# Performance work log

Measured on AMD Instinct MI355X. Metric: run time of the kernel, lower is better.

The kernel has to match this reference:

```python
import jax, jax.numpy as jnp
import numpy as np

# Module dims (match init_kwargs / input_specs)
V = 25        # number of graph nodes (chain skeleton)
K = 3         # max receptive-field size (neighbors incl. self), padded
CIN = 64
COUT = 64
N = 16
T = 512
TK = 3        # temporal_kernel
PAD = TK // 2 # time_pad default


def _build_graph():
    # Chain adjacency with self-links: node i <-> {i-1, i, i+1}
    A = np.zeros((V, V), np.float32)
    for i in range(V):
        A[i, i] = 1.0
        if i > 0:
            A[i, i - 1] = 1.0
        if i < V - 1:
            A[i, i + 1] = 1.0
    # Pad each node's neighbor list to K entries; mask marks real neighbors.
    idx = np.zeros((V, K), np.int32)
    mask = np.zeros((V, K), bool)
    for i in range(V):
        nb = np.where(A[i] != 0)[0]
        idx[i, : len(nb)] = nb
        mask[i, : len(nb)] = True
    return idx, mask


def setup_inputs() -> dict:
    key = jax.random.key(0)
    k_x, k_w, k_b = jax.random.split(key, 3)
    x = jax.random.normal(k_x, (N, CIN, V, T), dtype=jnp.float32)
    # One Conv2d kernel per node: [V, C_out, C_in, K, TK]; padded neighbor
    # slots are zeroed via mask inside reference().
    W = jax.random.normal(k_w, (V, COUT, CIN, K, TK), dtype=jnp.float32) * 0.05
    b = jax.random.normal(k_b, (V, COUT), dtype=jnp.float32) * 0.05
    idx_np, mask_np = _build_graph()
    return {
        "x": x,
        "W": W,
        "b": b,
        "idx": jnp.asarray(idx_np),
        "mask": jnp.asarray(mask_np),
    }


def reference(x, W, b, idx, mask):
    # x: [N, C, V, T]; W: [V, O, C, K, TK]; b: [V, O]; idx/mask: [V, K]
    Tt = x.shape[-1]
    # Zero out padded neighbor slots so padded rows contribute nothing
    # (equivalent to torch's variable-height per-node kernels).
    Wm = jnp.where(mask[:, None, None, :, None], W, 0.0)
    # Temporal zero padding (Conv2d padding=(0, time_pad))
    xp = jnp.pad(x, ((0, 0), (0, 0), (0, 0), (PAD, PAD)))
    # Batched neighbor gather: [N, C, V, K, T + 2*PAD]
    g = xp[:, :, idx, :]
    # Cross-correlation over the TK temporal taps (stride 1)
    out = jnp.zeros((x.shape[0], W.shape[1], V, Tt), dtype=x.dtype)
    for kt in range(TK):
        out = out + jnp.einsum(
            "ncvkt,vock->novt", g[..., kt : kt + Tt], Wm[..., kt]
        )
    out = out + b.T[None, :, :, None]  # per-node bias [O, V]
    return out
```

## Files before the change

### kernel.cpp

```cpp
#include <hip/hip_runtime.h>
#include <hip/hip_bf16.h>

#define NB   16
#define CINC 64
#define COUTC 64
#define NV   25
#define TLEN 512
#define KK   3
#define TKK  3

typedef short short8 __attribute__((ext_vector_type(8)));
typedef float f32x4  __attribute__((ext_vector_type(4)));
typedef float f32x16 __attribute__((ext_vector_type(16)));

#define XT_ROWS 514
#define XS_STRIDE 17408
#define NWT3BLK (NV * 9)

__device__ __forceinline__ unsigned pack_bf16(float lo, float hi) {
  __hip_bfloat16 l = __float2bfloat16(lo);
  __hip_bfloat16 h = __float2bfloat16(hi);
  unsigned short ul = *reinterpret_cast<unsigned short*>(&l);
  unsigned short uh = *reinterpret_cast<unsigned short*>(&h);
  return (unsigned)ul | ((unsigned)uh << 16);
}

__global__ __launch_bounds__(256) void prep_all(
    const float* __restrict__ x, const float* __restrict__ W,
    const unsigned char* __restrict__ mask_raw,
    __hip_bfloat16* __restrict__ Wt3, __hip_bfloat16* __restrict__ xT) {
  __shared__ float ts[64][65];
  int bid = blockIdx.x;
  if (bid < NWT3BLK) {
    int blk = bid;
    int v = blk / 9, kkt = blk % 9, k = kkt / 3, kt = kkt % 3;
    const int* mi = (const int*)mask_raw;
    int ok = 1;
    for (int i = 0; i < 18; ++i) {
      int m = mi[i];
      if (m != 0 && m != 1) ok = 0;
    }
    int m = ok ? mi[v * KK + k] : (int)(mask_raw[v * KK + k] != 0);
    const float* Wv = W + (size_t)v * COUTC * CINC * 9;
    __hip_bfloat16* dst = Wt3 + (size_t)blk * 4096;
    for (int i = threadIdx.x; i < 4096; i += 256) {
      int e     = i & 7;
      int lane  = (i >> 3) & 63;
      int ks    = (i >> 9) & 3;
      int oslab = i >> 11;
      int o = oslab * 32 + (lane & 31);
      int c = ks * 16 + 8 * (lane >> 5) + e;
      float val = m ? Wv[(o * CINC + c) * 9 + k * 3 + kt] : 0.f;
      dst[i] = __float2bfloat16(val);
    }
    return;
  }
  bid -= NWT3BLK;
  const int tb = (bid & 7) * 64;
  const int vn = bid >> 3;
  const int v  = vn % NV;
  const int n  = vn / NV;
  const int tid = threadIdx.x;
  for (int i = tid; i < 1024; i += 256) {
    int c = i >> 4, tq = (i & 15) * 4;
    float4 val = *(const float4*)(x + (((size_t)n * CINC + c) * NV + v) * TLEN + tb + tq);
    ts[c][tq + 0] = val.x;
    ts[c][tq + 1] = val.y;
    ts[c][tq + 2] = val.z;
    ts[c][tq + 3] = val.w;
  }
  __syncthreads();
  unsigned* base = (unsigned*)(xT + ((size_t)(n * NV + v) * XT_ROWS) * CINC);
  for (int i = tid; i < 512; i += 256) {
    int c8 = i & 7, t = i >> 3;
    int c0 = c8 * 8;
    uint4 d;
    d.x = pack_bf16(ts[c0 + 0][t], ts[c0 + 1][t]);
    d.y = pack_bf16(ts[c0 + 2][t], ts[c0 + 3][t]);
    d.z = pack_bf16(ts[c0 + 4][t], ts[c0 + 5][t]);
    d.w = pack_bf16(ts[c0 + 6][t], ts[c0 + 7][t]);
    *(uint4*)(base + (size_t)(tb + 1 + t) * 32 + c8 * 4) = d;
  }
  if (tb == 0 && tid < 32) base[tid] = 0u;
  if (tb == TLEN - 64 && tid < 32) base[513 * 32 + tid] = 0u;
}

__device__ __forceinline__ const char* slab_base(const __hip_bfloat16* xT,
                                                 int n, int vk, int tb) {
  return (const char*)xT + ((size_t)(n * NV + vk) * XT_ROWS + tb) * 128;
}

__global__ __launch_bounds__(256, 2) void lcn_mfma32(
    const __hip_bfloat16* __restrict__ xT,
    const __hip_bfloat16* __restrict__ Wt3,
    const float* __restrict__ bias,
    const int* __restrict__ idx,
    float* __restrict__ out) {
  __shared__ char xs[KK][XS_STRIDE];
  __shared__ char xs_dummy[1024];

  const int b  = blockIdx.x;
  const int n  = b & 15;
  const int tc = (b >> 4) & 1;
  const int v  = b >> 5;
  const int tid  = threadIdx.x;
  const int lane = tid & 63;
  const int wave = tid >> 6;
  const int os   = wave & 1;
  const int th   = wave >> 1;
  const int hi   = lane >> 5;
  const int l31  = lane & 31;

#define STAGE_PHASE(TBP)                                                      \
  {                                                                           \
    const char* gbs[KK] = {                                                   \
        slab_base(xT, n, idx[v * KK + 0], (TBP)),                             \
        slab_base(xT, n, idx[v * KK + 1], (TBP)),                             \
        slab_base(xT, n, idx[v * KK + 2], (TBP))};                            \
    _Pragma("unroll") for (int s = 0; s < KK; ++s) {                          \
      const char* gb = gbs[s];                                                \
      _Pragma("unroll") for (int q = 0; q < 4; ++q) {                         \
        int c = wave + q * 4;                                                 \
        int Lb = c * 1024 + lane * 16;                                        \
        int g = Lb ^ (((Lb >> 7) & 7) << 4);                                  \
        __builtin_amdgcn_global_load_lds(                                     \
            (const __attribute__((address_space(1))) void*)(gb + g),          \
            (__attribute__((address_space(3))) void*)(&xs[s][c * 1024]),      \
            16, 0, 0);                                                        \
      }                                                                       \
      if (wave == 0) {                                                        \
        int Lb = 16 * 1024 + lane * 16;                                       \
        int g = Lb ^ (((Lb >> 7) & 7) << 4);                                  \
        __builtin_amdgcn_global_load_lds(                                     \
            (const __attribute__((address_space(1))) void*)(gb + g),          \
            (__attribute__((address_space(3))) void*)(&xs[s][16 * 1024]),     \
            16, 0, 0);                                                        \
      } else {                                                                \
        __builtin_amdgcn_global_load_lds(                                     \
            (const __attribute__((address_space(1))) void*)(gb + lane * 16),  \
            (__attribute__((address_space(3))) void*)(xs_dummy),              \
            16, 0, 0);                                                        \
      }                                                                       \
      __builtin_amdgcn_sched_barrier(0);                                      \
    }                                                                         \
  }

#define COMPUTE_K(CB, KB)                                                     \
  _Pragma("unroll") for (int kt = 0; kt < TKK; ++kt) {                        \
    {                                                                         \
      const int r  = th * 64 + l31 + kt;                                      \
      const int sw = (r & 7) << 4;                                            \
      const int co = hi * 16;                                                 \
      const char* bp = (CB) + r * 128;                                        \
      _Pragma("unroll") for (int ks = 0; ks < 4; ++ks) {                      \
        short8 bfr = *(const short8*)(bp + ((co + 32 * ks) ^ sw));            \
        acc0 = __builtin_amdgcn_mfma_f32_32x32x16_bf16(                       \
            aA[((KB) + kt) * 4 + ks], bfr, acc0, 0, 0, 0);                    \
      }                                                                       \
    }                                                                         \
    {                                                                         \
      const int r  = th * 64 + 32 + l31 + kt;                                 \
      const int sw = (r & 7) << 4;                                            \
      const int co = hi * 16;                                                 \
      const char* bp = (CB) + r * 128;                                        \
      _Pragma("unroll") for (int ks = 0; ks < 4; ++ks) {                      \
        short8 bfr = *(const short8*)(bp + ((co + 32 * ks) ^ sw));            \
        acc1 = __builtin_amdgcn_mfma_f32_32x32x16_bf16(                       \
            aA[((KB) + kt) * 4 + ks], bfr, acc1, 0, 0, 0);                    \
      }                                                                       \
    }                                                                         \
  }

#define STORES(PHB)                                                           \
  {                                                                           \
    const float* bv = bias + v * COUTC;                                       \
    _Pragma("unroll") for (int s = 0; s < 2; ++s) {                           \
      const f32x16& acc = s ? acc1 : acc0;                                    \
      const int t = (PHB) + th * 64 + s * 32 + l31;                           \
      _Pragma("unroll") for (int reg = 0; reg < 16; ++reg) {                  \
        int o = os * 32 + 4 * hi + (reg & 3) + 8 * (reg >> 2);                \
        out[(((size_t)n * COUTC + o) * NV + v) * TLEN + t] = acc[reg] + bv[o];\
      }                                                                       \
    }                                                                         \
  }

  short8 aA[36];
  {
    const short8* wb = (const short8*)Wt3 + ((size_t)(v * 9) * 2 + os) * 256 + lane;
#pragma unroll
    for (int bq = 0; bq < 9; ++bq)
#pragma unroll
      for (int ks = 0; ks < 4; ++ks)
        aA[bq * 4 + ks] = wb[bq * 512 + (ks << 6)];
  }
  __builtin_amdgcn_sched_barrier(0);
  const int tb0 = tc * 256;
  STAGE_PHASE(tb0)

  f32x16 acc0 = {}, acc1 = {};

  asm volatile("s_waitcnt vmcnt(10)" ::: "memory");
  __builtin_amdgcn_s_barrier();
  __builtin_amdgcn_sched_barrier(0);
  COMPUTE_K(xs[0], 0)

  asm volatile("s_waitcnt vmcnt(5)" ::: "memory");
  __builtin_amdgcn_s_barrier();
  __builtin_amdgcn_sched_barrier(0);
  COMPUTE_K(xs[1], 3)

  asm volatile("s_waitcnt vmcnt(0)" ::: "memory");
  __builtin_amdgcn_s_barrier();
  __builtin_amdgcn_sched_barrier(0);
  COMPUTE_K(xs[2], 6)

  __builtin_amdgcn_s_barrier();
  __builtin_amdgcn_sched_barrier(0);
  STAGE_PHASE(tb0 + 128)
  __builtin_amdgcn_sched_barrier(0);
  STORES(tb0)
  __builtin_amdgcn_sched_barrier(0);
  acc0 = (f32x16){};
  acc1 = (f32x16){};

  asm volatile("s_waitcnt vmcnt(42)" ::: "memory");
  __builtin_amdgcn_s_barrier();
  __builtin_amdgcn_sched_barrier(0);
  COMPUTE_K(xs[0], 0)

  asm volatile("s_waitcnt vmcnt(37)" ::: "memory");
  __builtin_amdgcn_s_barrier();
  __builtin_amdgcn_sched_barrier(0);
  COMPUTE_K(xs[1], 3)

  asm volatile("s_waitcnt vmcnt(32)" ::: "memory");
  __builtin_amdgcn_s_barrier();
  __builtin_amdgcn_sched_barrier(0);
  COMPUTE_K(xs[2], 6)

  STORES(tb0 + 128)

#undef STAGE_PHASE
#undef COMPUTE_K
#undef STORES
}

__global__ void prep_mask_kernel(const int* __restrict__ mask_raw,
                                 int* __restrict__ mask_out) {
  __shared__ int fmt;
  if (threadIdx.x == 0) {
    int ok = 1;
    for (int i = 0; i < 18; ++i) {
      int m = mask_raw[i];
      if (m != 0 && m != 1) ok = 0;
    }
    fmt = ok;
  }
  __syncthreads();
  int i = threadIdx.x;
  if (i < NV * KK) {
    int m;
    if (fmt) m = mask_raw[i];
    else     m = (((const unsigned char*)mask_raw)[i] != 0) ? 1 : 0;
    mask_out[i] = m;
  }
}

__global__ void prep_wt_kernel(const float* __restrict__ W,
                               float* __restrict__ Wt) {
  int v   = blockIdx.x / 9;
  int kkt = blockIdx.x % 9;
  const float* Wv = W + (size_t)v * COUTC * CINC * 9;
  float* dst = Wt + (size_t)blockIdx.x * (CINC * COUTC);
  for (int i = threadIdx.x; i < CINC * COUTC; i += 256) {
    int c = i >> 6;
    int o = i & 63;
    dst[i] = Wv[(o * CINC + c) * 9 + kkt];
  }
}

__global__ __launch_bounds__(256, 4) void lcn_main(
    const float* __restrict__ x, const float* __restrict__ Wt,
    const float* __restrict__ b, const int* __restrict__ idx,
    const int* __restrict__ maskn, float* __restrict__ out) {
  __shared__ float xsf[CINC][66];
  __shared__ float wsh[CINC][COUTC];
  const int tb  = blockIdx.x * 64;
  const int v   = blockIdx.y;
  const int n   = blockIdx.z;
  const int tid = threadIdx.x;
  const int t0  = tid & 63;
  const int og  = tid >> 6;
  float acc[16];
#pragma unroll
  for (int j = 0; j < 16; ++j) acc[j] = 0.f;
  for (int k = 0; k < KK; ++k) {
    const int vk = idx[v * KK + k];
    const int mk = maskn[v * KK + k];
    __syncthreads();
    for (int i = tid; i < CINC * 66; i += 256) {
      int c  = i / 66;
      int tt = i - c * 66;
      int gt = tb - 1 + tt;
      float val = 0.f;
      if (mk && gt >= 0 && gt < TLEN)
        val = x[(((size_t)n * CINC + c) * NV + vk) * TLEN + gt];
      xsf[c][tt] = val;
    }
    for (int kt = 0; kt < TKK; ++kt) {
      __syncthreads();
      const float4* src =
          (const float4*)(Wt + ((size_t)(v * KK + k) * TKK + kt) * (CINC * COUTC));
      for (int i = tid; i < CINC * COUTC / 4; i += 256)
        ((float4*)wsh)[i] = src[i];
      __syncthreads();
#pragma unroll 4
      for (int c = 0; c < CINC; ++c) {
        float xv = xsf[c][t0 + kt];
        const float4* wrow = (const float4*)&wsh[c][og * 16];
#pragma unroll
        for (int j4 = 0; j4 < 4; ++j4) {
          float4 wv = wrow[j4];
          acc[j4 * 4 + 0] = fmaf(wv.x, xv, acc[j4 * 4 + 0]);
          acc[j4 * 4 + 1] = fmaf(wv.y, xv, acc[j4 * 4 + 1]);
          acc[j4 * 4 + 2] = fmaf(wv.z, xv, acc[j4 * 4 + 2]);
          acc[j4 * 4 + 3] = fmaf(wv.w, xv, acc[j4 * 4 + 3]);
        }
      }
    }
  }
#pragma unroll
  for (int j = 0; j < 16; ++j) {
    int o = og * 16 + j;
    out[(((size_t)n * COUTC + o) * NV + v) * TLEN + tb + t0] =
        acc[j] + b[v * COUTC + o];
  }
}

extern "C" void kernel_launch(void* const* d_in, const int* in_sizes, int n_in,
                              void* d_out, int out_size, void* d_ws, size_t ws_size,
                              hipStream_t stream) {
  const float* x    = (const float*)d_in[0];
  const float* W    = (const float*)d_in[1];
  const float* b    = (const float*)d_in[2];
  const int*   idx  = (const int*)d_in[3];
  const void*  mask = (const void*)d_in[4];
  float* out = (float*)d_out;

  const size_t WT3_BYTES = (size_t)NV * 9 * 4096 * sizeof(__hip_bfloat16);
  const size_t XT_BYTES  = (size_t)NB * NV * XT_ROWS * CINC * sizeof(__hip_bfloat16);
  const size_t NEED      = 512 + WT3_BYTES + XT_BYTES + 2048;

  if (ws_size >= NEED) {
    __hip_bfloat16* Wt3 = (__hip_bfloat16*)((char*)d_ws + 512);
    __hip_bfloat16* xT  = (__hip_bfloat16*)((char*)d_ws + 512 + WT3_BYTES);
    hipLaunchKernelGGL(prep_all, dim3(NWT3BLK + 8 * NV * NB), dim3(256), 0,
                       stream, x, W, (const unsigned char*)mask, Wt3, xT);
    hipLaunchKernelGGL(lcn_mfma32, dim3(NB * 2 * NV), dim3(256), 0,
                       stream, xT, Wt3, b, idx, out);
  } else {
    int*   maskn = (int*)d_ws;
    float* Wt    = (float*)((char*)d_ws + 512);
    hipLaunchKernelGGL(prep_mask_kernel, dim3(1), dim3(128), 0, stream,
                       (const int*)mask, maskn);
    hipLaunchKernelGGL(prep_wt_kernel, dim3(NV * KK * TKK), dim3(256), 0, stream,
                       W, Wt);
    hipLaunchKernelGGL(lcn_main, dim3(TLEN / 64, NV, NB), dim3(256), 0, stream,
                       x, Wt, b, idx, maskn, out);
  }
}
```

Before: 56.14 us.

## Double-buffer per-neighbor weight fragments to cut VGPRs and raise occupancy to 3

Instead of holding all 36 weight fragments for the three neighbors in registers for the whole kernel, the kernel keeps two 12-fragment buffers and reloads each neighbor's weights just before its compute phase, ping-ponging between them. Launch bounds are raised from 2 to 3 blocks per CU, and the vmcnt wait counts are retuned to cover the extra in-flight weight loads. The aim is lower register pressure and higher occupancy, so LDS staging and global loads overlap better. In exchange, weights are fetched twice per block, and the hand-tuned vmcnt counts must exactly match the issue order or the kernel will race.

```diff
diff --git a/kernel.cpp b/kernel.cpp
--- a/kernel.cpp
+++ b/kernel.cpp
@@ -90,7 +90,7 @@
   return (const char*)xT + ((size_t)(n * NV + vk) * XT_ROWS + tb) * 128;
 }
 
-__global__ __launch_bounds__(256, 2) void lcn_mfma32(
+__global__ __launch_bounds__(256, 3) void lcn_mfma32(
     const __hip_bfloat16* __restrict__ xT,
     const __hip_bfloat16* __restrict__ Wt3,
     const float* __restrict__ bias,
@@ -110,6 +110,15 @@
   const int th   = wave >> 1;
   const int hi   = lane >> 5;
   const int l31  = lane & 31;
+
+#define LOAD_A(DST, KIDX)                                                     \
+  {                                                                           \
+    const short8* wb = (const short8*)Wt3 +                                   \
+        ((size_t)((v * KK + (KIDX)) * TKK) * 2 + os) * 256 + lane;            \
+    _Pragma("unroll") for (int kt = 0; kt < TKK; ++kt)                        \
+      _Pragma("unroll") for (int ks = 0; ks < 4; ++ks)                        \
+        DST[kt * 4 + ks] = wb[kt * 512 + (ks << 6)];                          \
+  }
 
 #define STAGE_PHASE(TBP)                                                      \
   {                                                                           \
@@ -145,7 +154,7 @@
     }                                                                         \
   }
 
-#define COMPUTE_K(CB, KB)                                                     \
+#define COMPUTE_K(CB, A)                                                      \
   _Pragma("unroll") for (int kt = 0; kt < TKK; ++kt) {                        \
     {                                                                         \
       const int r  = th * 64 + l31 + kt;                                      \
@@ -154,8 +163,8 @@
       const char* bp = (CB) + r * 128;                                        \
       _Pragma("unroll") for (int ks = 0; ks < 4; ++ks) {                      \
         short8 bfr = *(const short8*)(bp + ((co + 32 * ks) ^ sw));            \
-        acc0 = __builtin_amdgcn_mfma_f32_32x32x16_bf16(                       \
-            aA[((KB) + kt) * 4 + ks], bfr, acc0, 0, 0, 0);                    \
+        acc0 = __builtin_amdgcn_mfma_f32_32x32x16_bf16(A[kt * 4 + ks], bfr,   \
+                                                       acc0, 0, 0, 0);        \
       }                                                                       \
     }                                                                         \
     {                                                                         \
@@ -165,8 +174,8 @@
       const char* bp = (CB) + r * 128;                                        \
       _Pragma("unroll") for (int ks = 0; ks < 4; ++ks) {                      \
         short8 bfr = *(const short8*)(bp + ((co + 32 * ks) ^ sw));            \
-        acc1 = __builtin_amdgcn_mfma_f32_32x32x16_bf16(                       \
-            aA[((KB) + kt) * 4 + ks], bfr, acc1, 0, 0, 0);                    \
+        acc1 = __builtin_amdgcn_mfma_f32_32x32x16_bf16(A[kt * 4 + ks], bfr,   \
+                                                       acc1, 0, 0, 0);        \
       }                                                                       \
     }                                                                         \
   }
@@ -184,37 +193,36 @@
     }                                                                         \
   }
 
-  short8 aA[36];
-  {
-    const short8* wb = (const short8*)Wt3 + ((size_t)(v * 9) * 2 + os) * 256 + lane;
-#pragma unroll
-    for (int bq = 0; bq < 9; ++bq)
-#pragma unroll
-      for (int ks = 0; ks < 4; ++ks)
-        aA[bq * 4 + ks] = wb[bq * 512 + (ks << 6)];
-  }
-  __builtin_amdgcn_sched_barrier(0);
   const int tb0 = tc * 256;
+  short8 aP[12], aQ[12];
+  f32x16 acc0 = {}, acc1 = {};
+
+  LOAD_A(aP, 0)
+  __builtin_amdgcn_sched_barrier(0);
   STAGE_PHASE(tb0)
 
-  f32x16 acc0 = {}, acc1 = {};
-
   asm volatile("s_waitcnt vmcnt(10)" ::: "memory");
   __builtin_amdgcn_s_barrier();
   __builtin_amdgcn_sched_barrier(0);
-  COMPUTE_K(xs[0], 0)
-
-  asm volatile("s_waitcnt vmcnt(5)" ::: "memory");
-  __builtin_amdgcn_s_barrier();
-  __builtin_amdgcn_sched_barrier(0);
-  COMPUTE_K(xs[1], 3)
-
-  asm volatile("s_waitcnt vmcnt(0)" ::: "memory");
-  __builtin_amdgcn_s_barrier();
-  __builtin_amdgcn_sched_barrier(0);
-  COMPUTE_K(xs[2], 6)
-
-  __builtin_amdgcn_s_barrier();
+  LOAD_A(aQ, 1)
+  __builtin_amdgcn_sched_barrier(0);
+  COMPUTE_K(xs[0], aP)
+
+  asm volatile("s_waitcnt vmcnt(17)" ::: "memory");
+  __builtin_amdgcn_s_barrier();
+  __builtin_amdgcn_sched_barrier(0);
+  LOAD_A(aP, 2)
+  __builtin_amdgcn_sched_barrier(0);
+  COMPUTE_K(xs[1], aQ)
+
+  asm volatile("s_waitcnt vmcnt(12)" ::: "memory");
+  __builtin_amdgcn_s_barrier();
+  __builtin_amdgcn_sched_barrier(0);
+  COMPUTE_K(xs[2], aP)
+
+  __builtin_amdgcn_s_barrier();
+  __builtin_amdgcn_sched_barrier(0);
+  LOAD_A(aQ, 0)
   __builtin_amdgcn_sched_barrier(0);
   STAGE_PHASE(tb0 + 128)
   __builtin_amdgcn_sched_barrier(0);
@@ -226,20 +234,25 @@
   asm volatile("s_waitcnt vmcnt(42)" ::: "memory");
   __builtin_amdgcn_s_barrier();
   __builtin_amdgcn_sched_barrier(0);
-  COMPUTE_K(xs[0], 0)
-
-  asm volatile("s_waitcnt vmcnt(37)" ::: "memory");
-  __builtin_amdgcn_s_barrier();
-  __builtin_amdgcn_sched_barrier(0);
-  COMPUTE_K(xs[1], 3)
-
-  asm volatile("s_waitcnt vmcnt(32)" ::: "memory");
-  __builtin_amdgcn_s_barrier();
-  __builtin_amdgcn_sched_barrier(0);
-  COMPUTE_K(xs[2], 6)
+  LOAD_A(aP, 1)
+  __builtin_amdgcn_sched_barrier(0);
+  COMPUTE_K(xs[0], aQ)
+
+  asm volatile("s_waitcnt vmcnt(49)" ::: "memory");
+  __builtin_amdgcn_s_barrier();
+  __builtin_amdgcn_sched_barrier(0);
+  LOAD_A(aQ, 2)
+  __builtin_amdgcn_sched_barrier(0);
+  COMPUTE_K(xs[1], aP)
+
+  asm volatile("s_waitcnt vmcnt(12)" ::: "memory");
+  __builtin_amdgcn_s_barrier();
+  __builtin_amdgcn_sched_barrier(0);
+  COMPUTE_K(xs[2], aQ)
 
   STORES(tb0 + 128)
 
+#undef LOAD_A
 #undef STAGE_PHASE
 #undef COMPUTE_K
 #undef STORES
```

New measurement: 83.02 us. +47.9%, slower.
